# Performance work log

Measured on AMD Instinct MI355X. Metric: run time of the kernel, lower is better.

The kernel has to match this reference:

```python
import jax, jax.numpy as jnp
import numpy as np

N, E = 30000, 600000
D_NODE, E_DIM, H1, H2, D_OUT = 128, 128, 256, 128, 128


def setup_inputs() -> dict:
    key = jax.random.key(0)
    ks = jax.random.split(key, 24)
    w = lambda k, shape: jax.random.normal(k, shape, jnp.float32) * 0.05
    return {
        "node_feat": jax.random.normal(ks[0], (N, D_NODE), jnp.float32),
        "src": jax.random.randint(ks[1], (E,), 0, N, jnp.int32),
        "dst": jax.random.randint(ks[2], (E,), 0, N, jnp.int32),
        "W_e1": w(ks[3], (2 * D_NODE + E_DIM, H1)), "b_e1": w(ks[4], (H1,)),
        "W_e2": w(ks[5], (H1, E_DIM)), "b_e2": w(ks[6], (E_DIM,)),
        "W_n1": w(ks[7], (D_NODE + E_DIM, H1)), "b_n1": w(ks[8], (H1,)),
        "W_n2": w(ks[9], (H1, H2)), "b_n2": w(ks[10], (H2,)),
        "W_el1": w(ks[11], (2 * H2, H1)), "b_el1": w(ks[12], (H1,)),
        "W_el2": w(ks[13], (H1, E_DIM)), "b_el2": w(ks[14], (E_DIM,)),
        "W_logit": w(ks[15], (E_DIM, 2)), "b_logit": w(ks[16], (2,)),
        "W_nro": w(ks[17], (H2, D_OUT)), "b_nro": w(ks[18], (D_OUT,)),
        "W_ero": w(ks[19], (E_DIM, D_OUT)), "b_ero": w(ks[20], (D_OUT,)),
        "msg_passing_steps": 2,
    }


def reference(node_feat, src, dst,
              W_e1, b_e1, W_e2, b_e2,
              W_n1, b_n1, W_n2, b_n2,
              W_el1, b_el1, W_el2, b_el2,
              W_logit, b_logit, W_nro, b_nro, W_ero, b_ero,
              msg_passing_steps):
    n_nodes = node_feat.shape[0]
    edge_dim = W_e2.shape[1]
    # incoming messages 'h', initialized to zeros
    h = jnp.zeros((n_nodes, edge_dim), node_feat.dtype)
    for _ in range(msg_passing_steps):
        # apply_edges: edge_feat = fc_edge2(relu(fc_edge([h_src, nf_src, nf_dst])))
        inp = jnp.concatenate([h[src], node_feat[src], node_feat[dst]], axis=-1)  # [E, edge_dim+2*D]
        edge_feat = jax.nn.relu(inp @ W_e1 + b_e1) @ W_e2 + b_e2                   # [E, edge_dim]
        # update_all with fn.sum: scatter-sum messages into destination nodes
        h = jax.ops.segment_sum(edge_feat, dst, num_segments=n_nodes)
    # apply_nodes: node_feat <- fc_node2(relu(fc_node([node_feat, h])))
    nf = jax.nn.relu(jnp.concatenate([node_feat, h], axis=-1) @ W_n1 + b_n1) @ W_n2 + b_n2  # [N, H2]
    n_out = nf @ W_nro + b_nro
    # compute_edge_logits: symmetric edge MLP over updated node reps
    s, d = nf[src], nf[dst]
    edge_mlp = lambda x: jax.nn.relu(x @ W_el1 + b_el1) @ W_el2 + b_el2
    comb = edge_mlp(jnp.concatenate([s, d], axis=-1)) + edge_mlp(jnp.concatenate([d, s], axis=-1))
    e_out_readout = comb @ W_ero + b_ero
    e_out = comb @ W_logit + b_logit
    return n_out, e_out_readout, e_out
```

## Files before the change

### kernel.cpp

```cpp
#include <hip/hip_runtime.h>
#include <hip/hip_bf16.h>

typedef __bf16 bf16;
typedef unsigned short u16;
typedef bf16 bf16x8 __attribute__((ext_vector_type(8)));
typedef bf16 bf16x4 __attribute__((ext_vector_type(4)));
typedef float f32x4 __attribute__((ext_vector_type(4)));

constexpr int NN = 30000;
constexpr int NE = 600000;
constexpr int D  = 128;

__device__ inline f32x4 mfma16(bf16x8 a, bf16x8 b, f32x4 c) {
    return __builtin_amdgcn_mfma_f32_16x16x32_bf16(a, b, c, 0, 0, 0);
}
__device__ inline bf16x8 ld8(const bf16* p) {
    return *reinterpret_cast<const bf16x8*>(p);
}
__device__ inline bf16x8 cvt8(const float* p) {
    float4 v0 = reinterpret_cast<const float4*>(p)[0];
    float4 v1 = reinterpret_cast<const float4*>(p)[1];
    bf16x8 r;
    r[0] = (bf16)v0.x; r[1] = (bf16)v0.y; r[2] = (bf16)v0.z; r[3] = (bf16)v0.w;
    r[4] = (bf16)v1.x; r[5] = (bf16)v1.y; r[6] = (bf16)v1.z; r[7] = (bf16)v1.w;
    return r;
}
__device__ inline int swz512(int row, int byteInRow) {
    return row * 512 + (byteInRow ^ ((row & 15) << 4));
}

struct TMat { const float* src; bf16* dst; int K; int Nc; };
struct TPack { TMat m[12]; };

__global__ void transpose_cast_kernel(TPack p) {
    TMat mm = p.m[blockIdx.x];
    int total = mm.K * mm.Nc;
    for (int idx = blockIdx.y * blockDim.x + threadIdx.x; idx < total;
         idx += gridDim.y * blockDim.x) {
        int c = idx / mm.K;
        int k = idx - c * mm.K;
        mm.dst[idx] = (bf16)mm.src[k * mm.Nc + c];
    }
}

__global__ void fuse_kernel(const float* __restrict__ W_el2,
                            const float* __restrict__ W_ero,
                            const float* __restrict__ W_logit,
                            const float* __restrict__ b_el2,
                            const float* __restrict__ b_ero,
                            const float* __restrict__ b_logit,
                            bf16* __restrict__ W2eroT, bf16* __restrict__ W2lgT,
                            float* __restrict__ b2ero, float* __restrict__ b2lg) {
    int k = blockIdx.x;
    int c = threadIdx.x;
    if (c >= 144) return;
    if (k < 256) {
        if (c < 128) {
            float s = 0.f;
            for (int j = 0; j < 128; ++j) s += W_el2[k * 128 + j] * W_ero[j * 128 + c];
            W2eroT[c * 256 + k] = (bf16)s;
        } else {
            int cc = c - 128;
            float s = 0.f;
            if (cc < 2) for (int j = 0; j < 128; ++j) s += W_el2[k * 128 + j] * W_logit[j * 2 + cc];
            W2lgT[cc * 256 + k] = (bf16)s;
        }
    } else {
        if (c < 128) {
            float s = b_ero[c];
            for (int j = 0; j < 128; ++j) s += 2.f * b_el2[j] * W_ero[j * 128 + c];
            b2ero[c] = s;
        } else if (c < 130) {
            int cc = c - 128;
            float s = b_logit[cc];
            for (int j = 0; j < 128; ++j) s += 2.f * b_el2[j] * W_logit[j * 2 + cc];
            b2lg[cc] = s;
        }
    }
}

__global__ void hist_kernel(const int* __restrict__ dst, int* __restrict__ counts) {
    int e = blockIdx.x * blockDim.x + threadIdx.x;
    if (e < NE) atomicAdd(counts + dst[e], 1);
}

__global__ void scan_kernel(const int* __restrict__ counts, int* __restrict__ offsets,
                            int* __restrict__ cursor) {
    __shared__ int tmp[1024];
    __shared__ int base;
    if (threadIdx.x == 0) base = 0;
    __syncthreads();
    for (int c = 0; c < NN; c += 1024) {
        int i = c + threadIdx.x;
        int v = (i < NN) ? counts[i] : 0;
        tmp[threadIdx.x] = v;
        __syncthreads();
        for (int off = 1; off < 1024; off <<= 1) {
            int x = (threadIdx.x >= off) ? tmp[threadIdx.x - off] : 0;
            __syncthreads();
            tmp[threadIdx.x] += x;
            __syncthreads();
        }
        if (i < NN) {
            int excl = base + tmp[threadIdx.x] - v;
            offsets[i] = excl;
            cursor[i] = excl;
        }
        __syncthreads();
        if (threadIdx.x == 0) base += tmp[1023];
        __syncthreads();
    }
    if (threadIdx.x == 0) offsets[NN] = NE;
}

__global__ void scatter_kernel(const int* __restrict__ src, const int* __restrict__ dst,
                               int* __restrict__ cursor, int* __restrict__ perm,
                               u16* __restrict__ srcS, u16* __restrict__ dstS) {
    int e = blockIdx.x * blockDim.x + threadIdx.x;
    if (e < NE) {
        int d = dst[e];
        int p = atomicAdd(cursor + d, 1);
        perm[p] = e;
        srcS[p] = (u16)src[e];
        dstS[p] = (u16)d;
    }
}

template<bool IN_BF16>
__global__ void __launch_bounds__(256, 4)
node_pre_kernel(const float* __restrict__ inF, const bf16* __restrict__ inB,
                const bf16* __restrict__ WT,
                const float* __restrict__ bias0,
                bf16* __restrict__ O1, bf16* __restrict__ O2) {
    const int half = blockIdx.y;
    const int r0 = blockIdx.x * 64;
    const int t = threadIdx.x, wv = t >> 6, l = t & 63, lr = l & 15, qk = l >> 4;
    int row[4];
#pragma unroll
    for (int m = 0; m < 4; ++m) { int r = r0 + m * 16 + lr; row[m] = r < NN ? r : NN - 1; }
    int coln[4];
#pragma unroll
    for (int n = 0; n < 4; ++n) coln[n] = wv * 64 + n * 16 + lr;
    f32x4 acc[4][4];
#pragma unroll
    for (int m = 0; m < 4; ++m)
#pragma unroll
        for (int n = 0; n < 4; ++n) acc[m][n] = 0.f;
#pragma unroll
    for (int ks = 0; ks < 4; ++ks) {
        const int kg = ks * 32 + qk * 8;
        bf16x8 a[4], b[4];
#pragma unroll
        for (int m = 0; m < 4; ++m)
            a[m] = IN_BF16 ? ld8(inB + row[m] * D + kg) : cvt8(inF + row[m] * D + kg);
#pragma unroll
        for (int n = 0; n < 4; ++n) b[n] = ld8(WT + (half * 256 + coln[n]) * 128 + kg);
#pragma unroll
        for (int m = 0; m < 4; ++m)
#pragma unroll
            for (int n = 0; n < 4; ++n) acc[m][n] = mfma16(a[m], b[n], acc[m][n]);
    }
    bf16* O = half ? O2 : O1;
#pragma unroll
    for (int n = 0; n < 4; ++n) {
        float bia = (half == 0 && bias0) ? bias0[coln[n]] : 0.f;
#pragma unroll
        for (int m = 0; m < 4; ++m)
#pragma unroll
            for (int j = 0; j < 4; ++j) {
                int gr = r0 + m * 16 + qk * 4 + j;
                if (gr < NN) O[gr * 256 + coln[n]] = (bf16)(acc[m][n][j] + bia);
            }
    }
}

template<bool HBF>
__global__ void __launch_bounds__(256, 4)
s2_update_kernel(const void* __restrict__ h1, const bf16* __restrict__ WtopT,
                 bf16* __restrict__ S) {
    const int r0 = blockIdx.x * 64;
    const int t = threadIdx.x, wv = t >> 6, l = t & 63, lr = l & 15, qk = l >> 4;
    int row[4];
#pragma unroll
    for (int m = 0; m < 4; ++m) { int r = r0 + m * 16 + lr; row[m] = r < NN ? r : NN - 1; }
    int coln[4];
#pragma unroll
    for (int n = 0; n < 4; ++n) coln[n] = wv * 64 + n * 16 + lr;
    f32x4 acc[4][4];
#pragma unroll
    for (int m = 0; m < 4; ++m)
#pragma unroll
        for (int n = 0; n < 4; ++n) acc[m][n] = 0.f;
#pragma unroll
    for (int ks = 0; ks < 4; ++ks) {
        const int kg = ks * 32 + qk * 8;
        bf16x8 a[4], b[4];
#pragma unroll
        for (int m = 0; m < 4; ++m) {
            if constexpr (HBF) a[m] = ld8((const bf16*)h1 + row[m] * D + kg);
            else               a[m] = cvt8((const float*)h1 + row[m] * D + kg);
        }
#pragma unroll
        for (int n = 0; n < 4; ++n) b[n] = ld8(WtopT + coln[n] * 128 + kg);
#pragma unroll
        for (int m = 0; m < 4; ++m)
#pragma unroll
            for (int n = 0; n < 4; ++n) acc[m][n] = mfma16(a[m], b[n], acc[m][n]);
    }
#pragma unroll
    for (int n = 0; n < 4; ++n)
#pragma unroll
        for (int m = 0; m < 4; ++m)
#pragma unroll
            for (int j = 0; j < 4; ++j) {
                int gr = r0 + m * 16 + qk * 4 + j;
                if (gr < NN) {
                    int idx = gr * 256 + coln[n];
                    S[idx] = (bf16)((float)S[idx] + acc[m][n][j]);
                }
            }
}

__global__ void __launch_bounds__(256, 8)
seg_sum_kernel(const bf16* __restrict__ S, const bf16* __restrict__ Bm,
               const int* __restrict__ offsets, const u16* __restrict__ srcS,
               bf16* __restrict__ T) {
    const int gw = (blockIdx.x * blockDim.x + threadIdx.x) >> 6;
    if (gw >= NN) return;
    const int l = threadIdx.x & 63;
    const int beg = offsets[gw], end = offsets[gw + 1];
    bf16x4 bv = *reinterpret_cast<const bf16x4*>(Bm + (size_t)gw * 256 + l * 4);
    const float b0 = (float)bv[0], b1 = (float)bv[1], b2 = (float)bv[2], b3 = (float)bv[3];
    float t0 = 0.f, t1 = 0.f, t2 = 0.f, t3 = 0.f;
    int i = beg;
    for (; i + 2 <= end; i += 2) {
        int s0 = srcS[i];
        int s1 = srcS[i + 1];
        bf16x4 a0 = *reinterpret_cast<const bf16x4*>(S + (size_t)s0 * 256 + l * 4);
        bf16x4 a1 = *reinterpret_cast<const bf16x4*>(S + (size_t)s1 * 256 + l * 4);
        float v;
        v = (float)a0[0] + b0; t0 += v > 0.f ? v : 0.f;
        v = (float)a0[1] + b1; t1 += v > 0.f ? v : 0.f;
        v = (float)a0[2] + b2; t2 += v > 0.f ? v : 0.f;
        v = (float)a0[3] + b3; t3 += v > 0.f ? v : 0.f;
        v = (float)a1[0] + b0; t0 += v > 0.f ? v : 0.f;
        v = (float)a1[1] + b1; t1 += v > 0.f ? v : 0.f;
        v = (float)a1[2] + b2; t2 += v > 0.f ? v : 0.f;
        v = (float)a1[3] + b3; t3 += v > 0.f ? v : 0.f;
    }
    if (i < end) {
        int s0 = srcS[i];
        bf16x4 a0 = *reinterpret_cast<const bf16x4*>(S + (size_t)s0 * 256 + l * 4);
        float v;
        v = (float)a0[0] + b0; t0 += v > 0.f ? v : 0.f;
        v = (float)a0[1] + b1; t1 += v > 0.f ? v : 0.f;
        v = (float)a0[2] + b2; t2 += v > 0.f ? v : 0.f;
        v = (float)a0[3] + b3; t3 += v > 0.f ? v : 0.f;
    }
    bf16x4 o;
    o[0] = (bf16)t0; o[1] = (bf16)t1; o[2] = (bf16)t2; o[3] = (bf16)t3;
    *reinterpret_cast<bf16x4*>(T + (size_t)gw * 256 + l * 4) = o;
}

__global__ void __launch_bounds__(256, 4)
h_gemm_kernel(const bf16* __restrict__ T, const bf16* __restrict__ We2T,
              const float* __restrict__ b_e2, const int* __restrict__ deg,
              bf16* __restrict__ h) {
    const int r0 = blockIdx.x * 64;
    const int t = threadIdx.x, wv = t >> 6, l = t & 63, lr = l & 15, qk = l >> 4;
    int row[4];
#pragma unroll
    for (int m = 0; m < 4; ++m) { int r = r0 + m * 16 + lr; row[m] = r < NN ? r : NN - 1; }
    int col2[2];
#pragma unroll
    for (int n = 0; n < 2; ++n) col2[n] = wv * 32 + n * 16 + lr;
    f32x4 acc[4][2];
#pragma unroll
    for (int m = 0; m < 4; ++m)
#pragma unroll
        for (int n = 0; n < 2; ++n) acc[m][n] = 0.f;
#pragma unroll
    for (int ks = 0; ks < 8; ++ks) {
        const int kg = ks * 32 + qk * 8;
        bf16x8 a[4], b[2];
#pragma unroll
        for (int m = 0; m < 4; ++m) a[m] = ld8(T + (size_t)row[m] * 256 + kg);
#pragma unroll
        for (int n = 0; n < 2; ++n) b[n] = ld8(We2T + col2[n] * 256 + kg);
#pragma unroll
        for (int m = 0; m < 4; ++m)
#pragma unroll
            for (int n = 0; n < 2; ++n) acc[m][n] = mfma16(a[m], b[n], acc[m][n]);
    }
#pragma unroll
    for (int n = 0; n < 2; ++n) {
        float bw = b_e2[col2[n]];
#pragma unroll
        for (int m = 0; m < 4; ++m)
#pragma unroll
            for (int j = 0; j < 4; ++j) {
                int gr = r0 + m * 16 + qk * 4 + j;
                if (gr < NN)
                    h[(size_t)gr * D + col2[n]] = (bf16)(acc[m][n][j] + (float)deg[gr] * bw);
            }
    }
}

template<bool HBF>
__global__ void __launch_bounds__(256, 2)
node_mlp_kernel(const float* __restrict__ node_feat,
                const void* __restrict__ h2,
                const bf16* __restrict__ Wn1T,
                const bf16* __restrict__ Wn2T,
                const float* __restrict__ b_n1,
                const float* __restrict__ b_n2,
                bf16* __restrict__ nf2_bf) {
    __shared__ __align__(16) char sH[64 * 512];
    const int t = threadIdx.x, wv = t >> 6, l = t & 63, lr = l & 15, qk = l >> 4;
    const int r0 = blockIdx.x * 64;
    int row[4];
#pragma unroll
    for (int m = 0; m < 4; ++m) { int r = r0 + m * 16 + lr; row[m] = r < NN ? r : NN - 1; }
    int coln[4];
#pragma unroll
    for (int n = 0; n < 4; ++n) coln[n] = wv * 64 + n * 16 + lr;
    f32x4 acc[4][4];
#pragma unroll
    for (int m = 0; m < 4; ++m)
#pragma unroll
        for (int n = 0; n < 4; ++n) acc[m][n] = 0.f;
#pragma unroll
    for (int ks = 0; ks < 4; ++ks) {
        const int kg = ks * 32 + qk * 8;
        bf16x8 a[4], b[4];
#pragma unroll
        for (int m = 0; m < 4; ++m) a[m] = cvt8(node_feat + (size_t)row[m] * D + kg);
#pragma unroll
        for (int n = 0; n < 4; ++n) b[n] = ld8(Wn1T + coln[n] * 256 + kg);
#pragma unroll
        for (int m = 0; m < 4; ++m)
#pragma unroll
            for (int n = 0; n < 4; ++n) acc[m][n] = mfma16(a[m], b[n], acc[m][n]);
#pragma unroll
        for (int m = 0; m < 4; ++m) {
            if constexpr (HBF) a[m] = ld8((const bf16*)h2 + (size_t)row[m] * D + kg);
            else               a[m] = cvt8((const float*)h2 + (size_t)row[m] * D + kg);
        }
#pragma unroll
        for (int n = 0; n < 4; ++n) b[n] = ld8(Wn1T + coln[n] * 256 + 128 + kg);
#pragma unroll
        for (int m = 0; m < 4; ++m)
#pragma unroll
            for (int n = 0; n < 4; ++n) acc[m][n] = mfma16(a[m], b[n], acc[m][n]);
    }
#pragma unroll
    for (int n = 0; n < 4; ++n) {
        float bia = b_n1[coln[n]];
#pragma unroll
        for (int m = 0; m < 4; ++m)
#pragma unroll
            for (int j = 0; j < 4; ++j) {
                int r = m * 16 + qk * 4 + j;
                float v = acc[m][n][j] + bia;
                v = v > 0.f ? v : 0.f;
                *reinterpret_cast<bf16*>(sH + swz512(r, coln[n] * 2)) = (bf16)v;
            }
    }
    __syncthreads();
    int col2[2];
#pragma unroll
    for (int n = 0; n < 2; ++n) col2[n] = wv * 32 + n * 16 + lr;
    f32x4 acc2[4][2];
#pragma unroll
    for (int m = 0; m < 4; ++m)
#pragma unroll
        for (int n = 0; n < 2; ++n) acc2[m][n] = 0.f;
#pragma unroll
    for (int ks = 0; ks < 8; ++ks) {
        const int k0 = ks * 32 + qk * 8;
        bf16x8 a[4], b[2];
#pragma unroll
        for (int m = 0; m < 4; ++m)
            a[m] = *reinterpret_cast<const bf16x8*>(sH + swz512(m * 16 + lr, k0 * 2));
#pragma unroll
        for (int n = 0; n < 2; ++n) b[n] = ld8(Wn2T + col2[n] * 256 + k0);
#pragma unroll
        for (int m = 0; m < 4; ++m)
#pragma unroll
            for (int n = 0; n < 2; ++n) acc2[m][n] = mfma16(a[m], b[n], acc2[m][n]);
    }
#pragma unroll
    for (int n = 0; n < 2; ++n) {
        float bia = b_n2[col2[n]];
#pragma unroll
        for (int m = 0; m < 4; ++m)
#pragma unroll
            for (int j = 0; j < 4; ++j) {
                int gr = r0 + m * 16 + qk * 4 + j;
                if (gr < NN) nf2_bf[(size_t)gr * D + col2[n]] = (bf16)(acc2[m][n][j] + bia);
            }
    }
}

__global__ void __launch_bounds__(256, 4)
edge_logit_sorted(const bf16* __restrict__ U, const bf16* __restrict__ V,
                  const int* __restrict__ perm, const u16* __restrict__ srcS,
                  const u16* __restrict__ dstS,
                  const bf16* __restrict__ W2eroT, const bf16* __restrict__ W2lgT,
                  const float* __restrict__ b2ero, const float* __restrict__ b2lg,
                  float* __restrict__ e_ro, float* __restrict__ e_lg) {
    __shared__ int s_e[128];
    __shared__ int s_s[128];
    __shared__ int s_d[128];
    const int t = threadIdx.x, wv = t >> 6, l = t & 63, lr = l & 15, qk = l >> 4;
    const int p0 = blockIdx.x * 128;
    if (t < 128) {
        int p = min(p0 + t, NE - 1);
        s_e[t] = perm[p];
        s_s[t] = (int)srcS[p];
        s_d[t] = (int)dstS[p];
    }
    __syncthreads();

    int is[2], id[2];
#pragma unroll
    for (int m = 0; m < 2; ++m) {
        int el = wv * 32 + m * 16 + lr;
        is[m] = s_s[el];
        id[m] = s_d[el];
    }
    f32x4 aro[2][8];
    f32x4 alg[2];
#pragma unroll
    for (int m = 0; m < 2; ++m) {
        alg[m] = 0.f;
#pragma unroll
        for (int n = 0; n < 8; ++n) aro[m][n] = 0.f;
    }
#pragma unroll
    for (int ks = 0; ks < 8; ++ks) {
        const int kg = ks * 32 + qk * 8;
        bf16x8 a[2];
#pragma unroll
        for (int m = 0; m < 2; ++m) {
            bf16x8 us = ld8(U + (size_t)is[m] * 256 + kg);
            bf16x8 vd = ld8(V + (size_t)id[m] * 256 + kg);
            bf16x8 ud = ld8(U + (size_t)id[m] * 256 + kg);
            bf16x8 vs = ld8(V + (size_t)is[m] * 256 + kg);
#pragma unroll
            for (int i = 0; i < 8; ++i) {
                float f1 = (float)us[i] + (float)vd[i]; f1 = f1 > 0.f ? f1 : 0.f;
                float f2 = (float)ud[i] + (float)vs[i]; f2 = f2 > 0.f ? f2 : 0.f;
                a[m][i] = (bf16)(f1 + f2);
            }
        }
#pragma unroll
        for (int n = 0; n < 8; ++n) {
            bf16x8 b = ld8(W2eroT + (n * 16 + lr) * 256 + kg);
#pragma unroll
            for (int m = 0; m < 2; ++m) aro[m][n] = mfma16(a[m], b, aro[m][n]);
        }
        bf16x8 blg = ld8(W2lgT + lr * 256 + kg);
#pragma unroll
        for (int m = 0; m < 2; ++m) alg[m] = mfma16(a[m], blg, alg[m]);
    }
#pragma unroll
    for (int n = 0; n < 8; ++n) {
        int col = n * 16 + lr;
        float bia = b2ero[col];
#pragma unroll
        for (int m = 0; m < 2; ++m)
#pragma unroll
            for (int j = 0; j < 4; ++j) {
                int el = wv * 32 + m * 16 + qk * 4 + j;
                e_ro[(size_t)s_e[el] * D + col] = aro[m][n][j] + bia;
            }
    }
    if (lr < 2) {
        float bia = b2lg[lr];
#pragma unroll
        for (int m = 0; m < 2; ++m)
#pragma unroll
            for (int j = 0; j < 4; ++j) {
                int el = wv * 32 + m * 16 + qk * 4 + j;
                e_lg[(size_t)s_e[el] * 2 + lr] = alg[m][j] + bia;
            }
    }
}

__global__ void __launch_bounds__(256, 4)
edge_msg_kernel(const bf16* __restrict__ S, const bf16* __restrict__ Bm,
                const int* __restrict__ src, const int* __restrict__ dst,
                const bf16* __restrict__ We2T,
                const float* __restrict__ b_e2,
                float* __restrict__ h_out) {
    __shared__ int s_src[128];
    __shared__ int s_dst[128];
    const int t = threadIdx.x, wv = t >> 6, l = t & 63, lr = l & 15, qk = l >> 4;
    const int e0 = blockIdx.x * 128;
    if (t < 128)      s_src[t] = src[min(e0 + t, NE - 1)];
    else              s_dst[t - 128] = dst[min(e0 + t - 128, NE - 1)];
    __syncthreads();
    const bf16* pS[2];
    const bf16* pB[2];
#pragma unroll
    for (int m = 0; m < 2; ++m) {
        int el = wv * 32 + m * 16 + lr;
        pS[m] = S + s_src[el] * 256;
        pB[m] = Bm + s_dst[el] * 256;
    }
    f32x4 acc[2][8];
#pragma unroll
    for (int m = 0; m < 2; ++m)
#pragma unroll
        for (int n = 0; n < 8; ++n) acc[m][n] = 0.f;
#pragma unroll
    for (int ks = 0; ks < 8; ++ks) {
        const int kg = ks * 32 + qk * 8;
        bf16x8 a[2];
#pragma unroll
        for (int m = 0; m < 2; ++m) {
            bf16x8 sa = ld8(pS[m] + kg);
            bf16x8 sb = ld8(pB[m] + kg);
#pragma unroll
            for (int i = 0; i < 8; ++i) {
                float f = (float)sa[i] + (float)sb[i];
                a[m][i] = (bf16)(f > 0.f ? f : 0.f);
            }
        }
#pragma unroll
        for (int n = 0; n < 8; ++n) {
            bf16x8 b = ld8(We2T + (n * 16 + lr) * 256 + kg);
#pragma unroll
            for (int m = 0; m < 2; ++m) acc[m][n] = mfma16(a[m], b, acc[m][n]);
        }
    }
#pragma unroll
    for (int n = 0; n < 8; ++n) {
        int col = n * 16 + lr;
        float bia = b_e2[col];
#pragma unroll
        for (int m = 0; m < 2; ++m)
#pragma unroll
            for (int j = 0; j < 4; ++j) {
                int el = wv * 32 + m * 16 + qk * 4 + j;
                if (e0 + el < NE)
                    atomicAdd(h_out + s_dst[el] * D + col, acc[m][n][j] + bia);
            }
    }
}

__global__ void __launch_bounds__(256, 4)
edge_logit_fast(const bf16* __restrict__ U, const bf16* __restrict__ V,
                const int* __restrict__ src, const int* __restrict__ dst,
                const bf16* __restrict__ W2eroT,
                const bf16* __restrict__ W2lgT,
                const float* __restrict__ b2ero, const float* __restrict__ b2lg,
                float* __restrict__ e_ro, float* __restrict__ e_lg) {
    __shared__ int s_src[128];
    __shared__ int s_dst[128];
    const int t = threadIdx.x, wv = t >> 6, l = t & 63, lr = l & 15, qk = l >> 4;
    const int e0 = blockIdx.x * 128;
    if (t < 128)      s_src[t] = src[min(e0 + t, NE - 1)];
    else              s_dst[t - 128] = dst[min(e0 + t - 128, NE - 1)];
    __syncthreads();
    int is[2], id[2];
#pragma unroll
    for (int m = 0; m < 2; ++m) {
        int el = wv * 32 + m * 16 + lr;
        is[m] = s_src[el];
        id[m] = s_dst[el];
    }
    f32x4 aro[2][8];
    f32x4 alg[2];
#pragma unroll
    for (int m = 0; m < 2; ++m) {
        alg[m] = 0.f;
#pragma unroll
        for (int n = 0; n < 8; ++n) aro[m][n] = 0.f;
    }
#pragma unroll
    for (int ks = 0; ks < 8; ++ks) {
        const int kg = ks * 32 + qk * 8;
        bf16x8 a[2];
#pragma unroll
        for (int m = 0; m < 2; ++m) {
            bf16x8 us = ld8(U + is[m] * 256 + kg);
            bf16x8 vd = ld8(V + id[m] * 256 + kg);
            bf16x8 ud = ld8(U + id[m] * 256 + kg);
            bf16x8 vs = ld8(V + is[m] * 256 + kg);
#pragma unroll
            for (int i = 0; i < 8; ++i) {
                float f1 = (float)us[i] + (float)vd[i]; f1 = f1 > 0.f ? f1 : 0.f;
                float f2 = (float)ud[i] + (float)vs[i]; f2 = f2 > 0.f ? f2 : 0.f;
                a[m][i] = (bf16)(f1 + f2);
            }
        }
#pragma unroll
        for (int n = 0; n < 8; ++n) {
            bf16x8 b = ld8(W2eroT + (n * 16 + lr) * 256 + kg);
#pragma unroll
            for (int m = 0; m < 2; ++m) aro[m][n] = mfma16(a[m], b, aro[m][n]);
        }
        bf16x8 blg = ld8(W2lgT + lr * 256 + kg);
#pragma unroll
        for (int m = 0; m < 2; ++m) alg[m] = mfma16(a[m], blg, alg[m]);
    }
#pragma unroll
    for (int n = 0; n < 8; ++n) {
        int col = n * 16 + lr;
        float bia = b2ero[col];
#pragma unroll
        for (int m = 0; m < 2; ++m)
#pragma unroll
            for (int j = 0; j < 4; ++j) {
                int el = wv * 32 + m * 16 + qk * 4 + j;
                int e = e0 + el;
                if (e < NE) e_ro[e * D + col] = aro[m][n][j] + bia;
            }
    }
    if (lr < 2) {
        float bia = b2lg[lr];
#pragma unroll
        for (int m = 0; m < 2; ++m)
#pragma unroll
            for (int j = 0; j < 4; ++j) {
                int el = wv * 32 + m * 16 + qk * 4 + j;
                int e = e0 + el;
                if (e < NE) e_lg[e * 2 + lr] = alg[m][j] + bia;
            }
    }
}

__global__ void __launch_bounds__(256, 4)
nro_kernel(const bf16* __restrict__ nf2_bf, const bf16* __restrict__ WnroT,
           const float* __restrict__ b_nro, float* __restrict__ n_out) {
    const int r0 = blockIdx.x * 64;
    const int t = threadIdx.x, wv = t >> 6, l = t & 63, lr = l & 15, qk = l >> 4;
    int row[4];
#pragma unroll
    for (int m = 0; m < 4; ++m) { int r = r0 + m * 16 + lr; row[m] = r < NN ? r : NN - 1; }
    int col2[2];
#pragma unroll
    for (int n = 0; n < 2; ++n) col2[n] = wv * 32 + n * 16 + lr;
    f32x4 acc[4][2];
#pragma unroll
    for (int m = 0; m < 4; ++m)
#pragma unroll
        for (int n = 0; n < 2; ++n) acc[m][n] = 0.f;
#pragma unroll
    for (int ks = 0; ks < 4; ++ks) {
        const int kg = ks * 32 + qk * 8;
        bf16x8 a[4], b[2];
#pragma unroll
        for (int m = 0; m < 4; ++m) a[m] = ld8(nf2_bf + (size_t)row[m] * D + kg);
#pragma unroll
        for (int n = 0; n < 2; ++n) b[n] = ld8(WnroT + col2[n] * 128 + kg);
#pragma unroll
        for (int m = 0; m < 4; ++m)
#pragma unroll
            for (int n = 0; n < 2; ++n) acc[m][n] = mfma16(a[m], b[n], acc[m][n]);
    }
#pragma unroll
    for (int n = 0; n < 2; ++n) {
        float bia = b_nro[col2[n]];
#pragma unroll
        for (int m = 0; m < 4; ++m)
#pragma unroll
            for (int j = 0; j < 4; ++j) {
                int gr = r0 + m * 16 + qk * 4 + j;
                if (gr < NN) n_out[(size_t)gr * D + col2[n]] = acc[m][n][j] + bia;
            }
    }
}

extern "C" void kernel_launch(void* const* d_in, const int* in_sizes, int n_in,
                              void* d_out, int out_size, void* d_ws, size_t ws_size,
                              hipStream_t stream) {
    const float* node_feat = (const float*)d_in[0];
    const int*   src   = (const int*)d_in[1];
    const int*   dst   = (const int*)d_in[2];
    const float* W_e1  = (const float*)d_in[3];
    const float* b_e1  = (const float*)d_in[4];
    const float* W_e2  = (const float*)d_in[5];
    const float* b_e2  = (const float*)d_in[6];
    const float* W_n1  = (const float*)d_in[7];
    const float* b_n1  = (const float*)d_in[8];
    const float* W_n2  = (const float*)d_in[9];
    const float* b_n2  = (const float*)d_in[10];
    const float* W_el1 = (const float*)d_in[11];
    const float* b_el1 = (const float*)d_in[12];
    const float* W_el2 = (const float*)d_in[13];
    const float* b_el2 = (const float*)d_in[14];
    const float* W_logit = (const float*)d_in[15];
    const float* b_logit = (const float*)d_in[16];
    const float* W_nro = (const float*)d_in[17];
    const float* b_nro = (const float*)d_in[18];
    const float* W_ero = (const float*)d_in[19];
    const float* b_ero = (const float*)d_in[20];

    char* ws = (char*)d_ws;
    bf16* wb = (bf16*)ws;
    bf16* WmbT   = wb;
    bf16* WtopT  = wb + 65536;
    bf16* We2T   = wb + 98304;
    bf16* Wn1T   = wb + 131072;
    bf16* Wn2T   = wb + 196608;
    bf16* WuvT   = wb + 229376;
    bf16* WnroT  = wb + 294912;
    bf16* W2eroT = wb + 311296;
    bf16* W2lgT  = wb + 344064;
    float* fb    = (float*)(ws + 928000);
    float* b2ero = fb;
    float* b2lg  = fb + 128;

    float* out   = (float*)d_out;
    float* n_out = out;
    float* e_ro  = out + 3840000;
    float* e_lg  = out + 80640000;

    TPack pk;
    pk.m[0]  = {W_e1 + 128 * 256, WmbT,              128, 256};
    pk.m[1]  = {W_e1 + 256 * 256, WmbT + 256 * 128,  128, 256};
    pk.m[2]  = {W_e1,             WtopT,             128, 256};
    pk.m[3]  = {W_e2,             We2T,              256, 128};
    pk.m[4]  = {W_n1,             Wn1T,              256, 256};
    pk.m[5]  = {W_n2,             Wn2T,              256, 128};
    pk.m[6]  = {W_el1,            WuvT,              128, 256};
    pk.m[7]  = {W_el1 + 128 * 256, WuvT + 256 * 128, 128, 256};
    pk.m[8]  = {W_nro,            WnroT,             128, 128};
    pk.m[9]  = {W_nro,            WnroT,             128, 128};
    pk.m[10] = {W_nro,            WnroT,             128, 128};
    pk.m[11] = {W_nro,            WnroT,             128, 128};

    const size_t NEED_NEW = 28888576;

    if (ws_size >= NEED_NEW) {
        char* eb = (char*)e_ro;
        bf16* S    = (bf16*)(eb);
        bf16* Bm   = (bf16*)(eb + 15360000);
        bf16* T    = (bf16*)(eb + 30720000);
        bf16* h1   = (bf16*)(eb + 46080000);
        bf16* h2   = (bf16*)(eb + 53760000);
        int* counts  = (int*)(eb + 61440000);
        int* offsets = (int*)(eb + 61560000);
        int* cursor  = (int*)(eb + 61680004);
        bf16* U    = (bf16*)n_out;
        bf16* nf2_bf = (bf16*)(ws + 1048576);
        bf16* Vbuf   = (bf16*)(ws + 8728576);
        int*  perm   = (int*)(ws + 24088576);
        u16*  srcS   = (u16*)(ws + 26488576);
        u16*  dstS   = (u16*)(ws + 27688576);

        transpose_cast_kernel<<<dim3(12, 40), 256, 0, stream>>>(pk);
        fuse_kernel<<<257, 160, 0, stream>>>(W_el2, W_ero, W_logit, b_el2, b_ero, b_logit,
                                             W2eroT, W2lgT, b2ero, b2lg);
        hipMemsetAsync(counts, 0, NN * 4, stream);
        hist_kernel<<<(NE + 255) / 256, 256, 0, stream>>>(dst, counts);
        scan_kernel<<<1, 1024, 0, stream>>>(counts, offsets, cursor);
        scatter_kernel<<<(NE + 255) / 256, 256, 0, stream>>>(src, dst, cursor,
                                                             perm, srcS, dstS);
        node_pre_kernel<false><<<dim3(469, 2), 256, 0, stream>>>(
            node_feat, nullptr, WmbT, b_e1, S, Bm);
        seg_sum_kernel<<<7500, 256, 0, stream>>>(S, Bm, offsets, srcS, T);
        h_gemm_kernel<<<469, 256, 0, stream>>>(T, We2T, b_e2, counts, h1);
        s2_update_kernel<true><<<469, 256, 0, stream>>>(h1, WtopT, S);
        seg_sum_kernel<<<7500, 256, 0, stream>>>(S, Bm, offsets, srcS, T);
        h_gemm_kernel<<<469, 256, 0, stream>>>(T, We2T, b_e2, counts, h2);
        node_mlp_kernel<true><<<469, 256, 0, stream>>>(
            node_feat, h2, Wn1T, Wn2T, b_n1, b_n2, nf2_bf);
        node_pre_kernel<true><<<dim3(469, 2), 256, 0, stream>>>(
            nullptr, nf2_bf, WuvT, b_el1, U, Vbuf);
        edge_logit_sorted<<<4688, 256, 0, stream>>>(
            U, Vbuf, perm, srcS, dstS, W2eroT, W2lgT, b2ero, b2lg, e_ro, e_lg);
        nro_kernel<<<469, 256, 0, stream>>>(nf2_bf, WnroT, b_nro, n_out);
    } else {
        bf16* nf2_bf = (bf16*)(ws + 1048576);
        bf16* Vbuf   = (bf16*)(ws + 9000000);
        float* h1f = n_out;
        bf16*  S   = (bf16*)e_ro;
        bf16*  Bm  = (bf16*)((char*)e_ro + 15360000);
        float* h2f = (float*)((char*)e_ro + 30720000);
        bf16*  U   = (bf16*)n_out;

        transpose_cast_kernel<<<dim3(12, 40), 256, 0, stream>>>(pk);
        fuse_kernel<<<257, 160, 0, stream>>>(W_el2, W_ero, W_logit, b_el2, b_ero, b_logit,
                                             W2eroT, W2lgT, b2ero, b2lg);
        hipMemsetAsync(h1f, 0, (size_t)NN * D * 4, stream);
        hipMemsetAsync(h2f, 0, (size_t)NN * D * 4, stream);
        node_pre_kernel<false><<<dim3(469, 2), 256, 0, stream>>>(
            node_feat, nullptr, WmbT, b_e1, S, Bm);
        edge_msg_kernel<<<4688, 256, 0, stream>>>(S, Bm, src, dst, We2T, b_e2, h1f);
        s2_update_kernel<false><<<469, 256, 0, stream>>>(h1f, WtopT, S);
        edge_msg_kernel<<<4688, 256, 0, stream>>>(S, Bm, src, dst, We2T, b_e2, h2f);
        node_mlp_kernel<false><<<469, 256, 0, stream>>>(
            node_feat, h2f, Wn1T, Wn2T, b_n1, b_n2, nf2_bf);
        node_pre_kernel<true><<<dim3(469, 2), 256, 0, stream>>>(
            nullptr, nf2_bf, WuvT, b_el1, U, Vbuf);
        edge_logit_fast<<<4688, 256, 0, stream>>>(
            U, Vbuf, src, dst, W2eroT, W2lgT, b2ero, b2lg, e_ro, e_lg);
        nro_kernel<<<469, 256, 0, stream>>>(nf2_bf, WnroT, b_nro, n_out);
    }
}
```

Before: 782.7 us.

## Use nontemporal loads/stores, single-pass chunked scan, raise edge_logit occupancy

Rewrites the single-block prefix scan so each thread serially sums a 30-element chunk and then runs one block-wide scan over the chunk totals, instead of looping over 30 block-wide scans. Adds nontemporal loads and stores in seg_sum and edge_logit for gathered rows and for scattered outputs, aiming to reduce cache pollution. Raises the occupancy hint for edge_logit_sorted from 4 to 8 blocks per CU, which may force register spilling. Nontemporal hints on gathered rows that are reused by other edges may instead lower cache hit rates.

Result: slower. 1.737 ms (+121.9%).

```diff
diff --git a/kernel.cpp b/kernel.cpp
--- a/kernel.cpp
+++ b/kernel.cpp
@@ -16,6 +16,12 @@
 }
 __device__ inline bf16x8 ld8(const bf16* p) {
     return *reinterpret_cast<const bf16x8*>(p);
+}
+__device__ inline bf16x8 ld8nt(const bf16* p) {
+    return __builtin_nontemporal_load(reinterpret_cast<const bf16x8*>(p));
+}
+__device__ inline bf16x4 ld4nt(const bf16* p) {
+    return __builtin_nontemporal_load(reinterpret_cast<const bf16x4*>(p));
 }
 __device__ inline bf16x8 cvt8(const float* p) {
     float4 v0 = reinterpret_cast<const float4*>(p)[0];
@@ -86,31 +92,37 @@
 
 __global__ void scan_kernel(const int* __restrict__ counts, int* __restrict__ offsets,
                             int* __restrict__ cursor) {
-    __shared__ int tmp[1024];
-    __shared__ int base;
-    if (threadIdx.x == 0) base = 0;
+    __shared__ int part[1024];
+    const int t = threadIdx.x;
+    const int base = t * 30;
+    int local[30];
+    int s = 0;
+#pragma unroll
+    for (int i = 0; i < 30; ++i) {
+        int idx = base + i;
+        int v = (idx < NN) ? counts[idx] : 0;
+        local[i] = s;
+        s += v;
+    }
+    part[t] = s;
     __syncthreads();
-    for (int c = 0; c < NN; c += 1024) {
-        int i = c + threadIdx.x;
-        int v = (i < NN) ? counts[i] : 0;
-        tmp[threadIdx.x] = v;
+    for (int off = 1; off < 1024; off <<= 1) {
+        int x = (t >= off) ? part[t - off] : 0;
         __syncthreads();
-        for (int off = 1; off < 1024; off <<= 1) {
-            int x = (threadIdx.x >= off) ? tmp[threadIdx.x - off] : 0;
-            __syncthreads();
-            tmp[threadIdx.x] += x;
-            __syncthreads();
-        }
-        if (i < NN) {
-            int excl = base + tmp[threadIdx.x] - v;
-            offsets[i] = excl;
-            cursor[i] = excl;
-        }
+        part[t] += x;
         __syncthreads();
-        if (threadIdx.x == 0) base += tmp[1023];
-        __syncthreads();
-    }
-    if (threadIdx.x == 0) offsets[NN] = NE;
+    }
+    int chunkExcl = (t == 0) ? 0 : part[t - 1];
+#pragma unroll
+    for (int i = 0; i < 30; ++i) {
+        int idx = base + i;
+        if (idx < NN) {
+            int excl = chunkExcl + local[i];
+            offsets[idx] = excl;
+            cursor[idx] = excl;
+        }
+    }
+    if (t == 0) offsets[NN] = NE;
 }
 
 __global__ void scatter_kernel(const int* __restrict__ src, const int* __restrict__ dst,
@@ -236,8 +248,8 @@
     for (; i + 2 <= end; i += 2) {
         int s0 = srcS[i];
         int s1 = srcS[i + 1];
-        bf16x4 a0 = *reinterpret_cast<const bf16x4*>(S + (size_t)s0 * 256 + l * 4);
-        bf16x4 a1 = *reinterpret_cast<const bf16x4*>(S + (size_t)s1 * 256 + l * 4);
+        bf16x4 a0 = ld4nt(S + (size_t)s0 * 256 + l * 4);
+        bf16x4 a1 = ld4nt(S + (size_t)s1 * 256 + l * 4);
         float v;
         v = (float)a0[0] + b0; t0 += v > 0.f ? v : 0.f;
         v = (float)a0[1] + b1; t1 += v > 0.f ? v : 0.f;
@@ -250,7 +262,7 @@
     }
     if (i < end) {
         int s0 = srcS[i];
-        bf16x4 a0 = *reinterpret_cast<const bf16x4*>(S + (size_t)s0 * 256 + l * 4);
+        bf16x4 a0 = ld4nt(S + (size_t)s0 * 256 + l * 4);
         float v;
         v = (float)a0[0] + b0; t0 += v > 0.f ? v : 0.f;
         v = (float)a0[1] + b1; t1 += v > 0.f ? v : 0.f;
@@ -259,7 +271,7 @@
     }
     bf16x4 o;
     o[0] = (bf16)t0; o[1] = (bf16)t1; o[2] = (bf16)t2; o[3] = (bf16)t3;
-    *reinterpret_cast<bf16x4*>(T + (size_t)gw * 256 + l * 4) = o;
+    __builtin_nontemporal_store(o, reinterpret_cast<bf16x4*>(T + (size_t)gw * 256 + l * 4));
 }
 
 __global__ void __launch_bounds__(256, 4)
@@ -402,7 +414,7 @@
     }
 }
 
-__global__ void __launch_bounds__(256, 4)
+__global__ void __launch_bounds__(256, 8)
 edge_logit_sorted(const bf16* __restrict__ U, const bf16* __restrict__ V,
                   const int* __restrict__ perm, const u16* __restrict__ srcS,
                   const u16* __restrict__ dstS,
@@ -443,10 +455,10 @@
         bf16x8 a[2];
 #pragma unroll
         for (int m = 0; m < 2; ++m) {
-            bf16x8 us = ld8(U + (size_t)is[m] * 256 + kg);
+            bf16x8 us = ld8nt(U + (size_t)is[m] * 256 + kg);
+            bf16x8 vs = ld8nt(V + (size_t)is[m] * 256 + kg);
+            bf16x8 ud = ld8(U + (size_t)id[m] * 256 + kg);
             bf16x8 vd = ld8(V + (size_t)id[m] * 256 + kg);
-            bf16x8 ud = ld8(U + (size_t)id[m] * 256 + kg);
-            bf16x8 vs = ld8(V + (size_t)is[m] * 256 + kg);
 #pragma unroll
             for (int i = 0; i < 8; ++i) {
                 float f1 = (float)us[i] + (float)vd[i]; f1 = f1 > 0.f ? f1 : 0.f;
@@ -473,7 +485,8 @@
 #pragma unroll
             for (int j = 0; j < 4; ++j) {
                 int el = wv * 32 + m * 16 + qk * 4 + j;
-                e_ro[(size_t)s_e[el] * D + col] = aro[m][n][j] + bia;
+                __builtin_nontemporal_store(aro[m][n][j] + bia,
+                                            e_ro + (size_t)s_e[el] * D + col);
             }
     }
     if (lr < 2) {
@@ -483,7 +496,8 @@
 #pragma unroll
             for (int j = 0; j < 4; ++j) {
                 int el = wv * 32 + m * 16 + qk * 4 + j;
-                e_lg[(size_t)s_e[el] * 2 + lr] = alg[m][j] + bia;
+                __builtin_nontemporal_store(alg[m][j] + bia,
+                                            e_lg + (size_t)s_e[el] * 2 + lr);
             }
     }
 }
```
